# Performance work log

Hardware: AMD Instinct MI355X
Metric: run time of the kernel (lower is better)

The kernel has to match this reference:

```python
import jax, jax.numpy as jnp
import numpy as np

B, S, T, DIN, DM, H = 4, 2048, 2048, 256, 512, 8
DH = DM // H
NEG = float(-2**32 + 1)
EPS = 1e-6


def layer_norm(x, g, b):
    mu = jnp.mean(x, axis=-1, keepdims=True)
    var = jnp.mean(jnp.square(x - mu), axis=-1, keepdims=True)
    return (x - mu) * jax.lax.rsqrt(var + EPS) * g + b


def mha(q_in, k_in, v_in, key_mask, wq, bq, wk, bk, wv, bv, w2, b2, g, beta, masked):
    b_, sq, _ = q_in.shape
    sk = k_in.shape[1]
    Q = (q_in @ wq + bq).reshape(b_, sq, H, DH)
    K = (k_in @ wk + bk).reshape(b_, sk, H, DH)
    V = (v_in @ wv + bv).reshape(b_, sk, H, DH)
    scores = jnp.einsum('bqhd,bkhd->bhqk', Q, K) / jnp.sqrt(jnp.float32(DH))
    if masked:
        m = key_mask.astype(jnp.float32).reshape(b_, 1, 1, sk)  # [B,1,1,Tk]
        scores = jnp.where(m == 0, jnp.float32(NEG), scores)
    attn = jax.nn.softmax(scores, axis=-1)  # dropout = identity at inference
    out = jnp.einsum('bhqk,bkhd->bqhd', attn, V).reshape(b_, sq, DM)
    out = out @ w2 + b2 + q_in
    return layer_norm(out, g, beta)


def setup_inputs() -> dict:
    key = jax.random.key(0)
    ks = jax.random.split(key, 16)
    w = lambda k, shp: (jax.random.normal(k, shp, jnp.float32) * 0.02)
    d = {
        'x': jax.random.normal(ks[0], (B, S, DIN), jnp.float32),
        'encoder_output': jax.random.normal(ks[1], (B, T, DIN), jnp.float32),
        'tgt_mask': jax.random.randint(ks[2], (B, S, 1), 0, 2, jnp.int32),
        'src_mask': jax.random.randint(ks[3], (B, T, 1), 0, 2, jnp.int32),
        'm1_wq': w(ks[4], (DIN, DM)), 'm1_bq': jnp.zeros((DM,), jnp.float32),
        'm1_wk': w(ks[5], (DIN, DM)), 'm1_bk': jnp.zeros((DM,), jnp.float32),
        'm1_wv': w(ks[6], (DIN, DM)), 'm1_bv': jnp.zeros((DM,), jnp.float32),
        'm1_w2': w(ks[7], (DM, DIN)), 'm1_b2': jnp.zeros((DIN,), jnp.float32),
        'm1_g': jnp.ones((DIN,), jnp.float32), 'm1_b': jnp.zeros((DIN,), jnp.float32),
        'm2_wq': w(ks[8], (DIN, DM)), 'm2_bq': jnp.zeros((DM,), jnp.float32),
        'm2_wk': w(ks[9], (DIN, DM)), 'm2_bk': jnp.zeros((DM,), jnp.float32),
        'm2_wv': w(ks[10], (DIN, DM)), 'm2_bv': jnp.zeros((DM,), jnp.float32),
        'm2_w2': w(ks[11], (DM, DIN)), 'm2_b2': jnp.zeros((DIN,), jnp.float32),
        'm2_g': jnp.ones((DIN,), jnp.float32), 'm2_b': jnp.zeros((DIN,), jnp.float32),
        'ln1_g': jnp.ones((DIN,), jnp.float32), 'ln1_b': jnp.zeros((DIN,), jnp.float32),
        'ln2_g': jnp.ones((DIN,), jnp.float32), 'ln2_b': jnp.zeros((DIN,), jnp.float32),
        'ln3_g': jnp.ones((DIN,), jnp.float32), 'ln3_b': jnp.zeros((DIN,), jnp.float32),
        'ffn_w1': w(ks[12], (DIN, DM)), 'ffn_b1': jnp.zeros((DM,), jnp.float32),
        'ffn_w2': w(ks[13], (DM, DIN)), 'ffn_b2': jnp.zeros((DIN,), jnp.float32),
    }
    return d


def reference(x, encoder_output, tgt_mask, src_mask,
              m1_wq, m1_bq, m1_wk, m1_bk, m1_wv, m1_bv, m1_w2, m1_b2, m1_g, m1_b,
              m2_wq, m2_bq, m2_wk, m2_bk, m2_wv, m2_bv, m2_w2, m2_b2, m2_g, m2_b,
              ln1_g, ln1_b, ln2_g, ln2_b, ln3_g, ln3_b,
              ffn_w1, ffn_b1, ffn_w2, ffn_b2):
    attn1 = mha(x, x, x, tgt_mask, m1_wq, m1_bq, m1_wk, m1_bk, m1_wv, m1_bv,
                m1_w2, m1_b2, m1_g, m1_b, masked=True)
    x = layer_norm(x + attn1, ln1_g, ln1_b)
    attn2 = mha(x, encoder_output, encoder_output, src_mask,
                m2_wq, m2_bq, m2_wk, m2_bk, m2_wv, m2_bv,
                m2_w2, m2_b2, m2_g, m2_b, masked=False)
    x = layer_norm(x + attn2, ln2_g, ln2_b)
    ffn_out = jax.nn.relu(x @ ffn_w1 + ffn_b1) @ ffn_w2 + ffn_b2
    return layer_norm(x + ffn_out, ln3_g, ln3_b)
```

## Files before the change

kernel.cpp:

```cpp
#include <hip/hip_runtime.h>
#include <hip/hip_bf16.h>

#define B_ 4
#define S_ 2048
#define DIN_ 256
#define DM_ 512
#define H_ 8
#define DH_ 64
#define M_ (B_*S_)

typedef short bf16x8 __attribute__((ext_vector_type(8)));
typedef float f32x4 __attribute__((ext_vector_type(4)));
typedef float f32x16 __attribute__((ext_vector_type(16)));
typedef int v2i __attribute__((ext_vector_type(2)));
typedef unsigned int u32;
typedef unsigned long long u64;

#define MFMA16(a,b,c) __builtin_amdgcn_mfma_f32_16x16x32_bf16((a),(b),(c),0,0,0)
#define MFMA32(a,b,c) __builtin_amdgcn_mfma_f32_32x32x16_bf16((a),(b),(c),0,0,0)

__device__ __forceinline__ unsigned short f2bf(float f) {
  union { float f; unsigned u; } v; v.f = f;
  unsigned r = v.u + 0x7fffu + ((v.u >> 16) & 1u);
  return (unsigned short)(r >> 16);
}
__device__ __forceinline__ f32x4 f32x4_zero() { f32x4 v = {0.f,0.f,0.f,0.f}; return v; }
__device__ __forceinline__ f32x16 f32x16_zero() {
  f32x16 v;
#pragma unroll
  for (int i = 0; i < 16; ++i) v[i] = 0.f;
  return v;
}
__device__ __forceinline__ u32 cvtpk_bf16(float lo, float hi) {
  u32 r; asm("v_cvt_pk_bf16_f32 %0, %1, %2" : "=v"(r) : "v"(lo), "v"(hi)); return r;
}
__device__ __forceinline__ float exp2_asm(float x) {
  float r; asm("v_exp_f32 %0, %1" : "=v"(r) : "v"(x)); return r;
}
__device__ __forceinline__ float max3f(float a, float b, float c) {
  return fmaxf(fmaxf(a, b), c);
}
__device__ __forceinline__ void gload_lds16(const void* g, void* l) {
  __builtin_amdgcn_global_load_lds((const __attribute__((address_space(1))) unsigned int*)g,
                                   (__attribute__((address_space(3))) unsigned int*)l,
                                   16, 0, 0);
}

__global__ void cast_bf16_kernel(const float* __restrict__ in,
                                 unsigned short* __restrict__ out, int n4) {
  int i = blockIdx.x * blockDim.x + threadIdx.x;
  if (i < n4) {
    float4 v = ((const float4*)in)[i];
    ushort4 o;
    o.x = f2bf(v.x); o.y = f2bf(v.y); o.z = f2bf(v.z); o.w = f2bf(v.w);
    ((ushort4*)out)[i] = o;
  }
}

struct WtDesc {
  const float* src[10];
  unsigned short* dst[10];
  int ks[10];
};
__global__ void prep_w_kernel(WtDesc d) {
  int m = blockIdx.y;
  int ks = d.ks[m];
  int K = 1 << ks;
  int N = 131072 >> ks;
  int i = blockIdx.x * 256 + threadIdx.x;
  int n = i >> ks, k = i & (K - 1);
  d.dst[m][i] = f2bf(d.src[m][(size_t)k * N + n]);
}

template<int K, bool RELU>
__global__ __launch_bounds__(256) void gemm_tiled_kernel(
    const unsigned short* __restrict__ A,
    const unsigned short* __restrict__ W0, const unsigned short* __restrict__ W1,
    const unsigned short* __restrict__ W2,
    const float* __restrict__ b0, const float* __restrict__ b1, const float* __restrict__ b2,
    unsigned short* __restrict__ o0, unsigned short* __restrict__ o1,
    unsigned short* __restrict__ o2, float scale0) {
  const int sel = blockIdx.y >> 2;
  const unsigned short* Wt = sel == 0 ? W0 : (sel == 1 ? W1 : W2);
  const float* bias = sel == 0 ? b0 : (sel == 1 ? b1 : b2);
  unsigned short* out = sel == 0 ? o0 : (sel == 1 ? o1 : o2);
  const float scale = sel == 0 ? scale0 : 1.f;

  const int tid = threadIdx.x;
  const int w = tid >> 6, l = tid & 63;
  const int lr = l & 15, lg = l >> 4;
  const int wr = w >> 1, wc = w & 1;
  const int r0 = blockIdx.x * 128;
  const int c0 = (blockIdx.y & 3) * 128;

  __shared__ __align__(16) unsigned short As[2][128 * 32];
  __shared__ __align__(16) unsigned short Bs[2][128 * 32];

  f32x4 acc[4][4];
#pragma unroll
  for (int m = 0; m < 4; ++m)
#pragma unroll
    for (int n = 0; n < 4; ++n) acc[m][n] = f32x4_zero();

  auto stage = [&](int buf, int k0) {
#pragma unroll
    for (int i = 0; i < 2; ++i) {
      int c = w * 128 + i * 64 + l;
      int row = c >> 2, sl = c & 3;
      gload_lds16(A + (size_t)(r0 + row) * K + k0 + sl * 8,
                  &As[buf][(w * 128 + i * 64) * 8]);
      gload_lds16(Wt + (size_t)(c0 + row) * K + k0 + sl * 8,
                  &Bs[buf][(w * 128 + i * 64) * 8]);
    }
  };

  stage(0, 0);
  __syncthreads();

  const int NT = K / 32;
  for (int t = 0; t < NT; ++t) {
    if (t + 1 < NT) stage((t + 1) & 1, (t + 1) * 32);
    const unsigned short* AB = &As[t & 1][0];
    const unsigned short* BB = &Bs[t & 1][0];
    bf16x8 af[4], bf[4];
#pragma unroll
    for (int m = 0; m < 4; ++m)
      af[m] = *(const bf16x8*)&AB[(wr * 64 + m * 16 + lr) * 32 + lg * 8];
#pragma unroll
    for (int n = 0; n < 4; ++n)
      bf[n] = *(const bf16x8*)&BB[(wc * 64 + n * 16 + lr) * 32 + lg * 8];
#pragma unroll
    for (int m = 0; m < 4; ++m)
#pragma unroll
      for (int n = 0; n < 4; ++n)
        acc[m][n] = MFMA16(af[m], bf[n], acc[m][n]);
    __syncthreads();
  }

#pragma unroll
  for (int n = 0; n < 4; ++n) {
    int col = c0 + wc * 64 + n * 16 + lr;
    float bv = bias[col];
#pragma unroll
    for (int m = 0; m < 4; ++m) {
#pragma unroll
      for (int r = 0; r < 4; ++r) {
        int row = r0 + wr * 64 + m * 16 + lg * 4 + r;
        float v = (acc[m][n][r] + bv) * scale;
        if (RELU) v = fmaxf(v, 0.f);
        out[(size_t)row * DM_ + col] = f2bf(v);
      }
    }
  }
}

template<int NLN>
__global__ __launch_bounds__(256) void gemm_ln_kernel(
    const unsigned short* __restrict__ A,
    const unsigned short* __restrict__ Wt,
    const float* __restrict__ bias,
    const float* __restrict__ res,
    const float* __restrict__ gA, const float* __restrict__ bA,
    const float* __restrict__ gB, const float* __restrict__ bB,
    float* __restrict__ outF,
    unsigned short* __restrict__ outB) {
  const int tid = threadIdx.x;
  const int w = tid >> 6, l = tid & 63;
  const int lr = l & 15, lg = l >> 4;
  const int wh = w & 1, wv = w >> 1;
  const int r0 = blockIdx.x * 32;

  __shared__ __align__(16) unsigned short Bs[2][256 * 32];
  __shared__ __align__(16) unsigned short As[2][32 * 32];
  __shared__ float ex[32][2][2];

  f32x4 acc[8];
#pragma unroll
  for (int n = 0; n < 8; ++n) acc[n] = f32x4_zero();

  auto stage = [&](int buf, int k0) {
#pragma unroll
    for (int i = 0; i < 4; ++i) {
      int c = w * 256 + i * 64 + l;
      int row = c >> 2, sl = c & 3;
      gload_lds16(Wt + (size_t)row * 512 + k0 + sl * 8,
                  &Bs[buf][(w * 256 + i * 64) * 8]);
    }
    if (w < 2) {
      int c = w * 64 + l;
      int row = c >> 2, sl = c & 3;
      gload_lds16(A + (size_t)(r0 + row) * 512 + k0 + sl * 8,
                  &As[buf][w * 64 * 8]);
    }
  };

  stage(0, 0);
  __syncthreads();

  for (int t = 0; t < 16; ++t) {
    if (t + 1 < 16) stage((t + 1) & 1, (t + 1) * 32);
    const unsigned short* BB = &Bs[t & 1][0];
    const unsigned short* AB = &As[t & 1][0];
    bf16x8 a = *(const bf16x8*)&AB[(wv * 16 + lr) * 32 + lg * 8];
#pragma unroll
    for (int n = 0; n < 8; ++n) {
      bf16x8 b = *(const bf16x8*)&BB[(wh * 128 + n * 16 + lr) * 32 + lg * 8];
      acc[n] = MFMA16(a, b, acc[n]);
    }
    __syncthreads();
  }

  f32x4 rv[8];
#pragma unroll
  for (int n = 0; n < 8; ++n) {
    int col = wh * 128 + n * 16 + lr;
    float bv = bias[col];
#pragma unroll
    for (int r = 0; r < 4; ++r) {
      int row = r0 + wv * 16 + lg * 4 + r;
      float rr = res[(size_t)row * 256 + col];
      rv[n][r] = rr;
      acc[n][r] += bv + rr;
    }
  }

  float mu[4], rs[4];
  {
    float s1[4], s2[4];
#pragma unroll
    for (int r = 0; r < 4; ++r) {
      float a1 = 0.f, a2 = 0.f;
#pragma unroll
      for (int n = 0; n < 8; ++n) { float v = acc[n][r]; a1 += v; a2 += v * v; }
#pragma unroll
      for (int off = 1; off < 16; off <<= 1) {
        a1 += __shfl_xor(a1, off);
        a2 += __shfl_xor(a2, off);
      }
      s1[r] = a1; s2[r] = a2;
    }
    if (lr == 0) {
#pragma unroll
      for (int r = 0; r < 4; ++r) {
        ex[wv * 16 + lg * 4 + r][wh][0] = s1[r];
        ex[wv * 16 + lg * 4 + r][wh][1] = s2[r];
      }
    }
    __syncthreads();
#pragma unroll
    for (int r = 0; r < 4; ++r) {
      int row = wv * 16 + lg * 4 + r;
      float t1 = ex[row][0][0] + ex[row][1][0];
      float t2 = ex[row][0][1] + ex[row][1][1];
      float m = t1 * (1.f / 256.f);
      float var = t2 * (1.f / 256.f) - m * m;
      mu[r] = m;
      rs[r] = rsqrtf(var + 1e-6f);
    }
  }

  if constexpr (NLN == 2) {
#pragma unroll
    for (int n = 0; n < 8; ++n) {
      int col = wh * 128 + n * 16 + lr;
      float g = gA[col], bb = bA[col];
#pragma unroll
      for (int r = 0; r < 4; ++r) {
        float t1 = (acc[n][r] - mu[r]) * rs[r] * g + bb;
        acc[n][r] = rv[n][r] + t1;
      }
    }
    float mu2[4], rs2[4];
    {
      float s1[4], s2[4];
#pragma unroll
      for (int r = 0; r < 4; ++r) {
        float a1 = 0.f, a2 = 0.f;
#pragma unroll
        for (int n = 0; n < 8; ++n) { float v = acc[n][r]; a1 += v; a2 += v * v; }
#pragma unroll
        for (int off = 1; off < 16; off <<= 1) {
          a1 += __shfl_xor(a1, off);
          a2 += __shfl_xor(a2, off);
        }
        s1[r] = a1; s2[r] = a2;
      }
      __syncthreads();
      if (lr == 0) {
#pragma unroll
        for (int r = 0; r < 4; ++r) {
          ex[wv * 16 + lg * 4 + r][wh][0] = s1[r];
          ex[wv * 16 + lg * 4 + r][wh][1] = s2[r];
        }
      }
      __syncthreads();
#pragma unroll
      for (int r = 0; r < 4; ++r) {
        int row = wv * 16 + lg * 4 + r;
        float t1 = ex[row][0][0] + ex[row][1][0];
        float t2 = ex[row][0][1] + ex[row][1][1];
        float m = t1 * (1.f / 256.f);
        float var = t2 * (1.f / 256.f) - m * m;
        mu2[r] = m;
        rs2[r] = rsqrtf(var + 1e-6f);
      }
    }
#pragma unroll
    for (int n = 0; n < 8; ++n) {
      int col = wh * 128 + n * 16 + lr;
      float g = gB[col], bb = bB[col];
#pragma unroll
      for (int r = 0; r < 4; ++r) {
        int row = r0 + wv * 16 + lg * 4 + r;
        float o = (acc[n][r] - mu2[r]) * rs2[r] * g + bb;
        outF[(size_t)row * 256 + col] = o;
        outB[(size_t)row * 256 + col] = f2bf(o);
      }
    }
  } else {
#pragma unroll
    for (int n = 0; n < 8; ++n) {
      int col = wh * 128 + n * 16 + lr;
      float g = gA[col], bb = bA[col];
#pragma unroll
      for (int r = 0; r < 4; ++r) {
        int row = r0 + wv * 16 + lg * 4 + r;
        float o = (acc[n][r] - mu[r]) * rs[r] * g + bb;
        outF[(size_t)row * 256 + col] = o;
      }
    }
  }
}

__global__ __launch_bounds__(256) void trans_kernel(const unsigned short* __restrict__ V,
                                                    unsigned short* __restrict__ Vt) {
  __shared__ __align__(16) unsigned short T[64][72];
  int v = threadIdx.x;
  int b = blockIdx.z;
  int s0 = blockIdx.x * 64, c0 = blockIdx.y * 64;
#pragma unroll
  for (int it = 0; it < 2; ++it) {
    int r = (v >> 3) + it * 32, c8 = (v & 7) * 8;
    *(bf16x8*)&T[r][c8] = *(const bf16x8*)&V[((size_t)b * S_ + s0 + r) * DM_ + c0 + c8];
  }
  __syncthreads();
#pragma unroll
  for (int it = 0; it < 2; ++it) {
    int cr = (v >> 3) + it * 32, s8 = (v & 7) * 8;
    bf16x8 o;
#pragma unroll
    for (int j = 0; j < 8; ++j) o[j] = (short)T[s8 + j][cr];
    *(bf16x8*)&Vt[((size_t)b * DM_ + c0 + cr) * S_ + s0 + s8] = o;
  }
}

template<bool MASKED>
__global__ __launch_bounds__(256) void flash_kernel(
    const unsigned short* __restrict__ Q,
    const unsigned short* __restrict__ Kg,
    const unsigned short* __restrict__ Vt,
    const int* __restrict__ mask,
    unsigned short* __restrict__ O) {
  __shared__ __align__(16) unsigned short lds[2][2][64 * 64];
  const int tid = threadIdx.x;
  const int w = tid >> 6, l = tid & 63;
  const int q32 = l & 31, hi = l >> 5;
  const int b = blockIdx.z, h = blockIdx.y;
  const size_t bS = (size_t)b * S_;
  const int q0 = blockIdx.x * 128 + w * 32;

  bf16x8 qf[4];
  {
    const unsigned short* qp = Q + (bS + q0 + q32) * DM_ + h * DH_;
#pragma unroll
    for (int c = 0; c < 4; ++c) qf[c] = *(const bf16x8*)(qp + c * 16 + hi * 8);
  }
  bf16x8 ones;
#pragma unroll
  for (int j = 0; j < 8; ++j) ones[j] = (short)0x3F80;

  f32x16 o0 = f32x16_zero(), o1 = f32x16_zero();
  float m = -1e30f, lsum = 0.f;

  auto stage = [&](int buf, int kv0) {
#pragma unroll
    for (int p = 0; p < 2; ++p) {
      int i = w * 2 + p;
      int row = i * 8 + (l >> 3);
      int slot = l & 7;
      gload_lds16(Kg + (bS + kv0 + row) * DM_ + h * DH_ + ((slot ^ (row & 7)) * 8),
                  &lds[buf][0][i * 8 * 64]);
      gload_lds16(Vt + ((size_t)b * DM_ + h * DH_ + row) * S_ + kv0 + ((slot ^ (row & 7)) * 8),
                  &lds[buf][1][i * 8 * 64]);
    }
  };

  stage(0, 0);
  int mvCur = 1;
  if (MASKED) mvCur = mask[bS + l];
  __syncthreads();

  const int NT = S_ / 64;
  for (int t = 0; t < NT; ++t) {
    int mvNext = 1;
    if (t + 1 < NT) {
      stage((t + 1) & 1, (t + 1) * 64);
      if (MASKED) mvNext = mask[bS + (t + 1) * 64 + l];
    }
    u64 bits = 0;
    if (MASKED) bits = __ballot(mvCur != 0);

    const unsigned short* KB = &lds[t & 1][0][0];
    const unsigned short* VB = &lds[t & 1][1][0];

    f32x16 sc[2];
    __builtin_amdgcn_s_setprio(1);
#pragma unroll
    for (int kt = 0; kt < 2; ++kt) {
      f32x16 s = f32x16_zero();
#pragma unroll
      for (int c = 0; c < 4; ++c) {
        int row = kt * 32 + q32;
        int slot = (c * 2 + hi) ^ (row & 7);
        bf16x8 kf = *(const bf16x8*)&KB[row * 64 + slot * 8];
        s = MFMA32(kf, qf[c], s);
      }
      if (MASKED) {
        u32 valid = (u32)(bits >> (kt * 32 + q32)) & 1u;
        u32 mfw = valid ? 0u : 0xC080C080u;
        union { u32 u[4]; bf16x8 v; } mf;
        mf.u[0] = mfw; mf.u[1] = mfw; mf.u[2] = mfw; mf.u[3] = mfw;
        s = MFMA32(mf.v, ones, s);
      }
      sc[kt] = s;
    }
    __builtin_amdgcn_s_setprio(0);

    float tm;
    {
      float r01;
#pragma unroll
      for (int kt = 0; kt < 2; ++kt) {
        float m0 = max3f(sc[kt][0], sc[kt][1], sc[kt][2]);
        float m1 = max3f(sc[kt][3], sc[kt][4], sc[kt][5]);
        float m2 = max3f(sc[kt][6], sc[kt][7], sc[kt][8]);
        float m3 = max3f(sc[kt][9], sc[kt][10], sc[kt][11]);
        float m4 = max3f(sc[kt][12], sc[kt][13], sc[kt][14]);
        float r = fmaxf(max3f(max3f(m0, m1, m2), m3, m4), sc[kt][15]);
        if (kt == 0) r01 = r; else r01 = fmaxf(r01, r);
      }
      tm = fmaxf(r01, __shfl_xor(r01, 32));
    }

    if (__any(tm > m + 11.5f)) {
      float mn = fmaxf(m, tm);
      float fac = exp2_asm(m - mn);
      m = mn;
      lsum *= fac;
#pragma unroll
      for (int i = 0; i < 16; ++i) {
        int rq = (i & 3) + 8 * (i >> 2) + 4 * hi;
        float fr = __shfl(fac, rq);
        o0[i] *= fr;
        o1[i] *= fr;
      }
    }

    float pv[2][16];
#pragma unroll
    for (int kt = 0; kt < 2; ++kt)
#pragma unroll
      for (int i = 0; i < 16; ++i) pv[kt][i] = exp2_asm(sc[kt][i] - m);

    {
      float s0 = 0.f, s1 = 0.f, s2 = 0.f, s3 = 0.f;
#pragma unroll
      for (int kt = 0; kt < 2; ++kt)
#pragma unroll
        for (int i = 0; i < 16; i += 4) {
          s0 += pv[kt][i]; s1 += pv[kt][i + 1];
          s2 += pv[kt][i + 2]; s3 += pv[kt][i + 3];
        }
      float rsum = (s0 + s1) + (s2 + s3);
      rsum += __shfl_xor(rsum, 32);
      lsum += rsum;
    }

    u32 w8[2][8];
#pragma unroll
    for (int kt = 0; kt < 2; ++kt)
#pragma unroll
      for (int j = 0; j < 8; ++j)
        w8[kt][j] = cvtpk_bf16(pv[kt][2 * j], pv[kt][2 * j + 1]);

    __builtin_amdgcn_s_setprio(1);
#pragma unroll
    for (int kt = 0; kt < 2; ++kt) {
#pragma unroll
      for (int kc = 0; kc < 2; ++kc) {
        v2i r0 = __builtin_amdgcn_permlane32_swap((int)w8[kt][4 * kc + 0],
                                                  (int)w8[kt][4 * kc + 2], false, false);
        v2i r1 = __builtin_amdgcn_permlane32_swap((int)w8[kt][4 * kc + 1],
                                                  (int)w8[kt][4 * kc + 3], false, false);
        union { u32 u[4]; bf16x8 v; } af;
        af.u[0] = (u32)r0.x; af.u[1] = (u32)r1.x; af.u[2] = (u32)r0.y; af.u[3] = (u32)r1.y;
        {
          int row = q32;
          int slot = (kt * 4 + kc * 2 + hi) ^ (row & 7);
          bf16x8 vf = *(const bf16x8*)&VB[row * 64 + slot * 8];
          o0 = MFMA32(af.v, vf, o0);
        }
        {
          int row = 32 + q32;
          int slot = (kt * 4 + kc * 2 + hi) ^ (row & 7);
          bf16x8 vf = *(const bf16x8*)&VB[row * 64 + slot * 8];
          o1 = MFMA32(af.v, vf, o1);
        }
      }
    }
    __builtin_amdgcn_s_setprio(0);
    __syncthreads();
    mvCur = mvNext;
  }

#pragma unroll
  for (int i = 0; i < 16; ++i) {
    int rq = (i & 3) + 8 * (i >> 2) + 4 * hi;
    float ls = __shfl(lsum, rq);
    float inv = __builtin_amdgcn_rcpf(ls);
    int row = q0 + rq;
    O[(bS + row) * DM_ + h * DH_ + q32] = f2bf(o0[i] * inv);
    O[(bS + row) * DM_ + h * DH_ + 32 + q32] = f2bf(o1[i] * inv);
  }
}

extern "C" void kernel_launch(void* const* d_in, const int* in_sizes, int n_in,
                              void* d_out, int out_size, void* d_ws, size_t ws_size,
                              hipStream_t stream) {
  const float* x     = (const float*)d_in[0];
  const float* eo    = (const float*)d_in[1];
  const int*   tmask = (const int*)d_in[2];
  const float* m1_wq = (const float*)d_in[4];  const float* m1_bq = (const float*)d_in[5];
  const float* m1_wk = (const float*)d_in[6];  const float* m1_bk = (const float*)d_in[7];
  const float* m1_wv = (const float*)d_in[8];  const float* m1_bv = (const float*)d_in[9];
  const float* m1_w2 = (const float*)d_in[10]; const float* m1_b2 = (const float*)d_in[11];
  const float* m1_g  = (const float*)d_in[12]; const float* m1_b  = (const float*)d_in[13];
  const float* m2_wq = (const float*)d_in[14]; const float* m2_bq = (const float*)d_in[15];
  const float* m2_wk = (const float*)d_in[16]; const float* m2_bk = (const float*)d_in[17];
  const float* m2_wv = (const float*)d_in[18]; const float* m2_bv = (const float*)d_in[19];
  const float* m2_w2 = (const float*)d_in[20]; const float* m2_b2 = (const float*)d_in[21];
  const float* m2_g  = (const float*)d_in[22]; const float* m2_b  = (const float*)d_in[23];
  const float* ln1_g = (const float*)d_in[24]; const float* ln1_b = (const float*)d_in[25];
  const float* ln2_g = (const float*)d_in[26]; const float* ln2_b = (const float*)d_in[27];
  const float* ln3_g = (const float*)d_in[28]; const float* ln3_b = (const float*)d_in[29];
  const float* f_w1  = (const float*)d_in[30]; const float* f_b1  = (const float*)d_in[31];
  const float* f_w2  = (const float*)d_in[32]; const float* f_b2  = (const float*)d_in[33];

  char* ws = (char*)d_ws;
  size_t off = 0;
  auto alloc = [&](size_t bytes) -> void* {
    void* p = ws + off;
    off += (bytes + 255) & ~(size_t)255;
    return p;
  };
  unsigned short* wt[10];
  for (int i = 0; i < 10; ++i) wt[i] = (unsigned short*)alloc(131072 * 2);
  unsigned short* xb  = (unsigned short*)alloc((size_t)M_ * DIN_ * 2);
  unsigned short* eb  = (unsigned short*)alloc((size_t)M_ * DIN_ * 2);
  unsigned short* Qb  = (unsigned short*)alloc((size_t)M_ * DM_ * 2);
  unsigned short* Kb  = (unsigned short*)alloc((size_t)M_ * DM_ * 2);
  unsigned short* Vb  = (unsigned short*)alloc((size_t)M_ * DM_ * 2);
  unsigned short* AOb = (unsigned short*)alloc((size_t)M_ * DM_ * 2);
  float*          X1  = (float*)alloc((size_t)M_ * DIN_ * 4);
  unsigned short* X1b = (unsigned short*)alloc((size_t)M_ * DIN_ * 2);
  float*          X2  = (float*)alloc((size_t)M_ * DIN_ * 4);
  unsigned short* X2b = (unsigned short*)alloc((size_t)M_ * DIN_ * 2);
  unsigned short* Hb  = Qb;
  unsigned short* VtA = (unsigned short*)X2;
  unsigned short* VtB = xb;

  int n4 = M_ * DIN_ / 4;
  cast_bf16_kernel<<<n4 / 256, 256, 0, stream>>>(x, xb, n4);
  cast_bf16_kernel<<<n4 / 256, 256, 0, stream>>>(eo, eb, n4);

  WtDesc wd;
  const float* srcs[10] = {m1_wq, m1_wk, m1_wv, m1_w2, m2_wq, m2_wk, m2_wv, m2_w2, f_w1, f_w2};
  int kss[10]           = {8,     8,     8,     9,     8,     8,     8,     9,     8,    9};
  for (int i = 0; i < 10; ++i) { wd.src[i] = srcs[i]; wd.dst[i] = wt[i]; wd.ks[i] = kss[i]; }
  prep_w_kernel<<<dim3(512, 10), 256, 0, stream>>>(wd);

  dim3 tg(S_ / 64, DM_ / 64, B_);
  dim3 fg(S_ / 128, H_, B_);
  const float QSCALE = 0.125f * 1.44269504088896f;

  gemm_tiled_kernel<256, false><<<dim3(M_ / 128, 12), 256, 0, stream>>>(
      xb, wt[0], wt[1], wt[2], m1_bq, m1_bk, m1_bv, Qb, Kb, Vb, QSCALE);
  trans_kernel<<<tg, 256, 0, stream>>>(Vb, VtA);
  flash_kernel<true><<<fg, 256, 0, stream>>>(Qb, Kb, VtA, tmask, AOb);
  gemm_ln_kernel<2><<<M_ / 32, 256, 0, stream>>>(AOb, wt[3], m1_b2, x,
                                                 m1_g, m1_b, ln1_g, ln1_b, X1, X1b);
  gemm_tiled_kernel<256, false><<<dim3(M_ / 128, 4), 256, 0, stream>>>(
      X1b, wt[4], wt[4], wt[4], m2_bq, m2_bq, m2_bq, Qb, Qb, Qb, QSCALE);
  gemm_tiled_kernel<256, false><<<dim3(M_ / 128, 8), 256, 0, stream>>>(
      eb, wt[5], wt[6], wt[6], m2_bk, m2_bv, m2_bv, Kb, Vb, Vb, 1.f);
  trans_kernel<<<tg, 256, 0, stream>>>(Vb, VtB);
  flash_kernel<false><<<fg, 256, 0, stream>>>(Qb, Kb, VtB, nullptr, AOb);
  gemm_ln_kernel<2><<<M_ / 32, 256, 0, stream>>>(AOb, wt[7], m2_b2, X1,
                                                 m2_g, m2_b, ln2_g, ln2_b, X2, X2b);
  gemm_tiled_kernel<256, true><<<dim3(M_ / 128, 4), 256, 0, stream>>>(
      X2b, wt[8], wt[8], wt[8], f_b1, f_b1, f_b1, Hb, Hb, Hb, 1.f);
  gemm_ln_kernel<1><<<M_ / 32, 256, 0, stream>>>(Hb, wt[9], f_b2, X2,
                                                 ln3_g, ln3_b, nullptr, nullptr,
                                                 (float*)d_out, nullptr);
}
```

Baseline: 226.5 us.

## Double flash-attention KV tile to 128 and remap blocks for XCD locality

Result: slower. 253.8 us (+12.0%).

```diff
diff --git a/kernel.cpp b/kernel.cpp
--- a/kernel.cpp
+++ b/kernel.cpp
@@ -361,13 +361,16 @@
     const unsigned short* __restrict__ Vt,
     const int* __restrict__ mask,
     unsigned short* __restrict__ O) {
-  __shared__ __align__(16) unsigned short lds[2][2][64 * 64];
+  __shared__ __align__(16) unsigned short lds[2][2][128 * 64];
   const int tid = threadIdx.x;
   const int w = tid >> 6, l = tid & 63;
   const int q32 = l & 31, hi = l >> 5;
-  const int b = blockIdx.z, h = blockIdx.y;
+  const int id = blockIdx.x;
+  const int g = (id & 7) * 64 + (id >> 3);
+  const int bh = g >> 4, xblk = g & 15;
+  const int b = bh >> 3, h = bh & 7;
   const size_t bS = (size_t)b * S_;
-  const int q0 = blockIdx.x * 128 + w * 32;
+  const int q0 = xblk * 128 + w * 32;
 
   bf16x8 qf[4];
   {
@@ -384,39 +387,48 @@
 
   auto stage = [&](int buf, int kv0) {
 #pragma unroll
-    for (int p = 0; p < 2; ++p) {
-      int i = w * 2 + p;
+    for (int p = 0; p < 4; ++p) {
+      int i = w * 4 + p;
       int row = i * 8 + (l >> 3);
       int slot = l & 7;
       gload_lds16(Kg + (bS + kv0 + row) * DM_ + h * DH_ + ((slot ^ (row & 7)) * 8),
                   &lds[buf][0][i * 8 * 64]);
-      gload_lds16(Vt + ((size_t)b * DM_ + h * DH_ + row) * S_ + kv0 + ((slot ^ (row & 7)) * 8),
-                  &lds[buf][1][i * 8 * 64]);
+    }
+#pragma unroll
+    for (int p = 0; p < 4; ++p) {
+      int i = w * 4 + p;
+      int row = i * 4 + (l >> 4);
+      int slot = l & 15;
+      gload_lds16(Vt + ((size_t)b * DM_ + h * DH_ + row) * S_ + kv0 + ((slot ^ (row & 15)) * 8),
+                  &lds[buf][1][i * 4 * 128]);
     }
   };
 
   stage(0, 0);
-  int mvCur = 1;
-  if (MASKED) mvCur = mask[bS + l];
+  int mv0 = 1, mv1 = 1;
+  if (MASKED) { mv0 = mask[bS + l]; mv1 = mask[bS + 64 + l]; }
   __syncthreads();
 
-  const int NT = S_ / 64;
+  const int NT = S_ / 128;
   for (int t = 0; t < NT; ++t) {
-    int mvNext = 1;
+    int n0 = 1, n1 = 1;
     if (t + 1 < NT) {
-      stage((t + 1) & 1, (t + 1) * 64);
-      if (MASKED) mvNext = mask[bS + (t + 1) * 64 + l];
-    }
-    u64 bits = 0;
-    if (MASKED) bits = __ballot(mvCur != 0);
+      stage((t + 1) & 1, (t + 1) * 128);
+      if (MASKED) {
+        n0 = mask[bS + (t + 1) * 128 + l];
+        n1 = mask[bS + (t + 1) * 128 + 64 + l];
+      }
+    }
+    u64 bits0 = 0, bits1 = 0;
+    if (MASKED) { bits0 = __ballot(mv0 != 0); bits1 = __ballot(mv1 != 0); }
 
     const unsigned short* KB = &lds[t & 1][0][0];
     const unsigned short* VB = &lds[t & 1][1][0];
 
-    f32x16 sc[2];
+    f32x16 sc[4];
     __builtin_amdgcn_s_setprio(1);
 #pragma unroll
-    for (int kt = 0; kt < 2; ++kt) {
+    for (int kt = 0; kt < 4; ++kt) {
       f32x16 s = f32x16_zero();
 #pragma unroll
       for (int c = 0; c < 4; ++c) {
@@ -426,7 +438,8 @@
         s = MFMA32(kf, qf[c], s);
       }
       if (MASKED) {
-        u32 valid = (u32)(bits >> (kt * 32 + q32)) & 1u;
+        u64 bb = (kt < 2) ? bits0 : bits1;
+        u32 valid = (u32)(bb >> ((kt & 1) * 32 + q32)) & 1u;
         u32 mfw = valid ? 0u : 0xC080C080u;
         union { u32 u[4]; bf16x8 v; } mf;
         mf.u[0] = mfw; mf.u[1] = mfw; mf.u[2] = mfw; mf.u[3] = mfw;
@@ -438,18 +451,18 @@
 
     float tm;
     {
-      float r01;
-#pragma unroll
-      for (int kt = 0; kt < 2; ++kt) {
+      float rmax;
+#pragma unroll
+      for (int kt = 0; kt < 4; ++kt) {
         float m0 = max3f(sc[kt][0], sc[kt][1], sc[kt][2]);
         float m1 = max3f(sc[kt][3], sc[kt][4], sc[kt][5]);
         float m2 = max3f(sc[kt][6], sc[kt][7], sc[kt][8]);
         float m3 = max3f(sc[kt][9], sc[kt][10], sc[kt][11]);
         float m4 = max3f(sc[kt][12], sc[kt][13], sc[kt][14]);
         float r = fmaxf(max3f(max3f(m0, m1, m2), m3, m4), sc[kt][15]);
-        if (kt == 0) r01 = r; else r01 = fmaxf(r01, r);
-      }
-      tm = fmaxf(r01, __shfl_xor(r01, 32));
+        if (kt == 0) rmax = r; else rmax = fmaxf(rmax, r);
+      }
+      tm = fmaxf(rmax, __shfl_xor(rmax, 32));
     }
 
     if (__any(tm > m + 11.5f)) {
@@ -466,61 +479,56 @@
       }
     }
 
-    float pv[2][16];
-#pragma unroll
-    for (int kt = 0; kt < 2; ++kt)
-#pragma unroll
-      for (int i = 0; i < 16; ++i) pv[kt][i] = exp2_asm(sc[kt][i] - m);
-
+#pragma unroll
+    for (int kt = 0; kt < 4; ++kt)
+#pragma unroll
+      for (int i = 0; i < 16; ++i) sc[kt][i] = exp2_asm(sc[kt][i] - m);
     {
       float s0 = 0.f, s1 = 0.f, s2 = 0.f, s3 = 0.f;
 #pragma unroll
-      for (int kt = 0; kt < 2; ++kt)
+      for (int kt = 0; kt < 4; ++kt)
 #pragma unroll
         for (int i = 0; i < 16; i += 4) {
-          s0 += pv[kt][i]; s1 += pv[kt][i + 1];
-          s2 += pv[kt][i + 2]; s3 += pv[kt][i + 3];
+          s0 += sc[kt][i]; s1 += sc[kt][i + 1];
+          s2 += sc[kt][i + 2]; s3 += sc[kt][i + 3];
         }
       float rsum = (s0 + s1) + (s2 + s3);
       rsum += __shfl_xor(rsum, 32);
       lsum += rsum;
     }
 
-    u32 w8[2][8];
-#pragma unroll
-    for (int kt = 0; kt < 2; ++kt)
+    __builtin_amdgcn_s_setprio(1);
+#pragma unroll
+    for (int kt = 0; kt < 4; ++kt) {
+      u32 w8[8];
 #pragma unroll
       for (int j = 0; j < 8; ++j)
-        w8[kt][j] = cvtpk_bf16(pv[kt][2 * j], pv[kt][2 * j + 1]);
-
-    __builtin_amdgcn_s_setprio(1);
-#pragma unroll
-    for (int kt = 0; kt < 2; ++kt) {
+        w8[j] = cvtpk_bf16(sc[kt][2 * j], sc[kt][2 * j + 1]);
 #pragma unroll
       for (int kc = 0; kc < 2; ++kc) {
-        v2i r0 = __builtin_amdgcn_permlane32_swap((int)w8[kt][4 * kc + 0],
-                                                  (int)w8[kt][4 * kc + 2], false, false);
-        v2i r1 = __builtin_amdgcn_permlane32_swap((int)w8[kt][4 * kc + 1],
-                                                  (int)w8[kt][4 * kc + 3], false, false);
+        v2i r0 = __builtin_amdgcn_permlane32_swap((int)w8[4 * kc + 0],
+                                                  (int)w8[4 * kc + 2], false, false);
+        v2i r1 = __builtin_amdgcn_permlane32_swap((int)w8[4 * kc + 1],
+                                                  (int)w8[4 * kc + 3], false, false);
         union { u32 u[4]; bf16x8 v; } af;
         af.u[0] = (u32)r0.x; af.u[1] = (u32)r1.x; af.u[2] = (u32)r0.y; af.u[3] = (u32)r1.y;
         {
           int row = q32;
-          int slot = (kt * 4 + kc * 2 + hi) ^ (row & 7);
-          bf16x8 vf = *(const bf16x8*)&VB[row * 64 + slot * 8];
+          int sl = (kt * 4 + kc * 2 + hi) ^ (row & 15);
+          bf16x8 vf = *(const bf16x8*)&VB[row * 128 + sl * 8];
           o0 = MFMA32(af.v, vf, o0);
         }
         {
           int row = 32 + q32;
-          int slot = (kt * 4 + kc * 2 + hi) ^ (row & 7);
-          bf16x8 vf = *(const bf16x8*)&VB[row * 64 + slot * 8];
+          int sl = (kt * 4 + kc * 2 + hi) ^ (row & 15);
+          bf16x8 vf = *(const bf16x8*)&VB[row * 128 + sl * 8];
           o1 = MFMA32(af.v, vf, o1);
         }
       }
     }
     __builtin_amdgcn_s_setprio(0);
     __syncthreads();
-    mvCur = mvNext;
+    mv0 = n0; mv1 = n1;
   }
 
 #pragma unroll
@@ -590,13 +598,13 @@
   prep_w_kernel<<<dim3(512, 10), 256, 0, stream>>>(wd);
 
   dim3 tg(S_ / 64, DM_ / 64, B_);
-  dim3 fg(S_ / 128, H_, B_);
+  const int FG = (S_ / 128) * H_ * B_;
   const float QSCALE = 0.125f * 1.44269504088896f;
 
   gemm_tiled_kernel<256, false><<<dim3(M_ / 128, 12), 256, 0, stream>>>(
       xb, wt[0], wt[1], wt[2], m1_bq, m1_bk, m1_bv, Qb, Kb, Vb, QSCALE);
   trans_kernel<<<tg, 256, 0, stream>>>(Vb, VtA);
-  flash_kernel<true><<<fg, 256, 0, stream>>>(Qb, Kb, VtA, tmask, AOb);
+  flash_kernel<true><<<FG, 256, 0, stream>>>(Qb, Kb, VtA, tmask, AOb);
   gemm_ln_kernel<2><<<M_ / 32, 256, 0, stream>>>(AOb, wt[3], m1_b2, x,
                                                  m1_g, m1_b, ln1_g, ln1_b, X1, X1b);
   gemm_tiled_kernel<256, false><<<dim3(M_ / 128, 4), 256, 0, stream>>>(
@@ -604,7 +612,7 @@
   gemm_tiled_kernel<256, false><<<dim3(M_ / 128, 8), 256, 0, stream>>>(
       eb, wt[5], wt[6], wt[6], m2_bk, m2_bv, m2_bv, Kb, Vb, Vb, 1.f);
   trans_kernel<<<tg, 256, 0, stream>>>(Vb, VtB);
-  flash_kernel<false><<<fg, 256, 0, stream>>>(Qb, Kb, VtB, nullptr, AOb);
+  flash_kernel<false><<<FG, 256, 0, stream>>>(Qb, Kb, VtB, nullptr, AOb);
   gemm_ln_kernel<2><<<M_ / 32, 256, 0, stream>>>(AOb, wt[7], m2_b2, X1,
                                                  m2_g, m2_b, ln2_g, ln2_b, X2, X2b);
   gemm_tiled_kernel<256, true><<<dim3(M_ / 128, 4), 256, 0, stream>>>(
```
